# Performance work log

Hardware: AMD Instinct MI355X
Metric: run time of the kernel (lower is better)

The kernel has to match this reference:

```python
import jax, jax.numpy as jnp
import numpy as np

B, N, D, H, DH = 2, 2048, 1024, 16, 64  # batch, seq, dim, heads, dim_head


def setup_inputs() -> dict:
    key = jax.random.key(0)
    ks = jax.random.split(key, 5)
    x = jax.random.normal(ks[0], (B, N, D), dtype=jnp.float32)
    Wq = jax.random.normal(ks[1], (D, H * DH), dtype=jnp.float32) * 0.02
    Wk = jax.random.normal(ks[2], (D, H * DH), dtype=jnp.float32) * 0.02
    Wv = jax.random.normal(ks[3], (D, H * DH), dtype=jnp.float32) * 0.02
    Wo = jax.random.normal(ks[4], (H * DH, D), dtype=jnp.float32) * 0.02
    bo = jnp.zeros((D,), dtype=jnp.float32)
    return {"x": x, "Wq": Wq, "Wk": Wk, "Wv": Wv, "Wo": Wo, "bo": bo}


def reference(x, Wq, Wk, Wv, Wo, bo):
    b, n, _ = x.shape
    scale = DH ** -0.5
    q = (x @ Wq).reshape(b, n, H, DH)
    k = (x @ Wk).reshape(b, n, H, DH)
    v = (x @ Wv).reshape(b, n, H, DH)
    # ALiBi slopes: 1 / (256**(1/H))**(h+1), per get_alibi_slope
    base = (2.0 ** 8) ** (1.0 / H)
    slope = 1.0 / base ** jnp.arange(1, H + 1, dtype=jnp.float32)  # [H]
    pos = jnp.arange(n, dtype=jnp.float32)
    # q_bias=[slope, slope*i], k_bias=[-j, 1] -> dot = slope*(i-j)
    bias = slope[:, None, None] * (pos[:, None] - pos[None, :])  # [H, N, N]
    scores = jnp.einsum('bihd,bjhd->bhij', q, k) * scale + bias[None]
    causal = pos[:, None] >= pos[None, :]  # i >= j
    scores = jnp.where(causal[None, None], scores, jnp.float32(-1e30))
    attn = jax.nn.softmax(scores, axis=-1)
    out = jnp.einsum('bhij,bjhd->bihd', attn, v).reshape(b, n, H * DH)
    return out @ Wo + bo
```

## Files before the change

### kernel.cpp

```cpp
#include <hip/hip_runtime.h>
#include <hip/hip_bf16.h>


typedef __bf16 bf16x8 __attribute__((ext_vector_type(8)));
typedef float f32x4 __attribute__((ext_vector_type(4)));
typedef short s4 __attribute__((ext_vector_type(4)));
typedef unsigned short ushort_t;

#define MFMA_16x16x32(a, b, c) __builtin_amdgcn_mfma_f32_16x16x32_bf16(a, b, c, 0, 0, 0)
#define MFMA16(a, b, c) __builtin_amdgcn_mfma_f32_16x16x16bf16_1k(a, b, c, 0, 0, 0)

__device__ __forceinline__ ushort_t f2bf(float f) {
    __hip_bfloat16 h = __float2bfloat16(f);
    return __builtin_bit_cast(ushort_t, h);
}
__device__ __forceinline__ float bf2f(ushort_t u) {
    unsigned x = ((unsigned)u) << 16;
    return __builtin_bit_cast(float, x);
}

__device__ __forceinline__ void gl_lds16(const ushort_t* g, ushort_t* l) {
    __builtin_amdgcn_global_load_lds(
        (const __attribute__((address_space(1))) void*)g,
        (__attribute__((address_space(3))) void*)l, 16, 0, 0);
}

__device__ __forceinline__ unsigned detect_fp32(const void* wp) {
    const ushort_t* w = (const ushort_t*)wp;
    unsigned c = 0;
    #pragma unroll
    for (int i = 0; i < 128; ++i) c += (((w[i] >> 7) & 0xFF) >= 0x7F) ? 1u : 0u;
    return (c > 8) ? 1u : 0u;
}

__device__ __forceinline__ uint4 load8(const void* p, size_t idx, unsigned flag) {
    if (flag) {
        const float* f = (const float*)p + idx;
        float4 a = *(const float4*)f;
        float4 b = *(const float4*)(f + 4);
        ushort_t u[8] = { f2bf(a.x), f2bf(a.y), f2bf(a.z), f2bf(a.w),
                          f2bf(b.x), f2bf(b.y), f2bf(b.z), f2bf(b.w) };
        return *(uint4*)u;
    }
    return *(const uint4*)((const ushort_t*)p + idx);
}

struct Sched { unsigned short v[1024]; };
constexpr Sched make_sched() {
    Sched s{};
    int jc[16] = {1, 1, 2, 2, 3, 4, 6, 8, 12, 16, 23, 32, 32, 32, 32, 32};
    int sorted[1024] = {};
    int n = 0;
    for (int w = 32; w >= 1; --w) {
        for (int id = 0; id < 1024; ++id) {
            int bh = id & 31, qb = id >> 5;
            int cap = jc[bh & 15];
            int wi = (qb + 1 < cap) ? (qb + 1) : cap;
            if (wi == w) sorted[n++] = id;
        }
    }
    for (int r = 0; r < 4; ++r)
        for (int k = 0; k < 256; ++k)
            s.v[r * 256 + k] = (unsigned short)sorted[r * 256 + ((r & 1) ? (255 - k) : k)];
    return s;
}
__constant__ Sched g_sched = make_sched();

__global__ __launch_bounds__(256) void convert_x(
    const void* __restrict__ X, const void* __restrict__ Wq, const void* __restrict__ bo,
    ushort_t* __restrict__ Xc, ushort_t* __restrict__ boc)
{
    const unsigned flag = detect_fp32(Wq);
    const int blk = blockIdx.x;
    if (blk < 2048) {
        size_t idx = (size_t)blk * 2048 + (size_t)threadIdx.x * 8;
        *(uint4*)(Xc + idx) = load8(X, idx, flag);
    } else {
        size_t idx = (size_t)threadIdx.x * 8;
        if (idx < 1024) *(uint4*)(boc + idx) = load8(bo, idx, flag);
    }
}

__global__ __launch_bounds__(256) void transpose_w(
    const void* __restrict__ Wq, const void* __restrict__ Wk,
    const void* __restrict__ Wv, const void* __restrict__ Wo,
    ushort_t* __restrict__ WqT, ushort_t* __restrict__ WkT,
    ushort_t* __restrict__ WvT, ushort_t* __restrict__ WoT)
{
    __shared__ ushort_t T[64][72];
    const unsigned flag = detect_fp32(Wq);
    const int z = blockIdx.z;
    const void* W = (z == 0) ? Wq : ((z == 1) ? Wk : ((z == 2) ? Wv : Wo));
    ushort_t* WT = (z == 0) ? WqT : ((z == 1) ? WkT : ((z == 2) ? WvT : WoT));

    const int k0 = blockIdx.y * 64, n0 = blockIdx.x * 64;
    const int r = threadIdx.x >> 2, c = (threadIdx.x & 3) * 16;

    *(uint4*)&T[r][c]     = load8(W, (size_t)(k0 + r) * 1024 + n0 + c,     flag);
    *(uint4*)&T[r][c + 8] = load8(W, (size_t)(k0 + r) * 1024 + n0 + c + 8, flag);
    __syncthreads();
    ushort_t tmp[16];
    #pragma unroll
    for (int j = 0; j < 16; ++j) tmp[j] = T[c + j][r];
    *(uint4*)(WT + (size_t)(n0 + r) * 1024 + k0 + c)     = *(uint4*)&tmp[0];
    *(uint4*)(WT + (size_t)(n0 + r) * 1024 + k0 + c + 8) = *(uint4*)&tmp[8];
}

__global__ __launch_bounds__(256) void qkv_gemm(
    const ushort_t* __restrict__ X, const ushort_t* __restrict__ WqT,
    const ushort_t* __restrict__ WkT, const ushort_t* __restrict__ WvT,
    ushort_t* __restrict__ Q, ushort_t* __restrict__ K, ushort_t* __restrict__ Vt)
{
    __shared__ ushort_t As[128 * 32];
    __shared__ ushort_t Bs[128 * 32];

    const int z = blockIdx.z;
    const ushort_t* WT = (z == 0) ? WqT : ((z == 1) ? WkT : WvT);

    const int tid  = threadIdx.x;
    const int m0   = blockIdx.y * 128, n0 = blockIdx.x * 128;
    const int lane = tid & 63, wv = tid >> 6;
    const int quad = lane >> 4, l15 = lane & 15;
    const int wm = (wv & 1) * 64, wn = (wv >> 1) * 64;

    const int lrow = lane >> 2;
    const int schk = (lane & 3) ^ ((lane >> 3) & 3);
    const int ra0_ = wv * 16 + lrow;
    ushort_t* aB0 = As + wv * 512;
    ushort_t* aB1 = As + 2048 + wv * 512;
    ushort_t* bB0 = Bs + wv * 512;
    ushort_t* bB1 = Bs + 2048 + wv * 512;
    const int sp = quad ^ ((l15 >> 1) & 3);

    f32x4 acc[4][4] = {};

    for (int kt = 0; kt < 32; ++kt) {
        const int k0 = kt * 32;
        __syncthreads();
        gl_lds16(X  + (size_t)(m0 + ra0_)      * 1024 + k0 + schk * 8, aB0);
        gl_lds16(X  + (size_t)(m0 + 64 + ra0_) * 1024 + k0 + schk * 8, aB1);
        gl_lds16(WT + (size_t)(n0 + ra0_)      * 1024 + k0 + schk * 8, bB0);
        gl_lds16(WT + (size_t)(n0 + 64 + ra0_) * 1024 + k0 + schk * 8, bB1);
        __syncthreads();

        bf16x8 af[4], bfr[4];
        #pragma unroll
        for (int t = 0; t < 4; ++t) {
            af[t]  = *(const bf16x8*)(As + (wm + t * 16 + l15) * 32 + sp * 8);
            bfr[t] = *(const bf16x8*)(Bs + (wn + t * 16 + l15) * 32 + sp * 8);
        }
        #pragma unroll
        for (int mt = 0; mt < 4; ++mt)
            #pragma unroll
            for (int nt = 0; nt < 4; ++nt)
                acc[mt][nt] = MFMA_16x16x32(af[mt], bfr[nt], acc[mt][nt]);
    }

    #pragma unroll
    for (int mt = 0; mt < 4; ++mt) {
        #pragma unroll
        for (int nt = 0; nt < 4; ++nt) {
            if (z == 2) {
                int c  = n0 + wn + nt * 16 + l15;
                int h  = c >> 6, dh = c & 63;
                int mA = m0 + wm + mt * 16 + quad * 4;
                int b  = mA >> 11, nseq = mA & 2047;
                ushort_t pk[4];
                #pragma unroll
                for (int r = 0; r < 4; ++r) pk[r] = f2bf(acc[mt][nt][r]);
                *(ushort2*)(Vt + ((size_t)((b * 16 + h) * 64 + dh)) * 2048 + nseq)     = *(ushort2*)&pk[0];
                *(ushort2*)(Vt + ((size_t)((b * 16 + h) * 64 + dh)) * 2048 + nseq + 2) = *(ushort2*)&pk[2];
            } else {
                ushort_t* dst = (z == 0) ? Q : K;
                #pragma unroll
                for (int r = 0; r < 4; ++r) {
                    int m = m0 + wm + mt * 16 + quad * 4 + r;
                    int c = n0 + wn + nt * 16 + l15;
                    int b = m >> 11, nseq = m & 2047;
                    int h = c >> 6, dh = c & 63;
                    dst[((size_t)((b * 16 + h) * 2048 + nseq)) * 64 + dh] = f2bf(acc[mt][nt][r]);
                }
            }
        }
    }
}

__global__ __launch_bounds__(256) void attn_kernel(
    const ushort_t* __restrict__ Q, const ushort_t* __restrict__ K,
    const ushort_t* __restrict__ Vt, ushort_t* __restrict__ AO)
{
    __shared__ ushort_t Ks[64 * 72];
    __shared__ ushort_t Vs[64 * 72];

    const int tid  = threadIdx.x;
    const int wv   = tid >> 6, lane = tid & 63;
    const int quad = lane >> 4, l15 = lane & 15;
    const int item = g_sched.v[blockIdx.x];
    const int bh   = item & 31, h = bh & 15, b = bh >> 4;
    const int qb   = item >> 5;
    const int iw   = qb * 64 + wv * 16;
    const int i_   = iw + l15;

    const ushort_t* Qh = Q  + (size_t)bh * 2048 * 64;
    const ushort_t* Kh = K  + (size_t)bh * 2048 * 64;
    const ushort_t* Vh = Vt + (size_t)bh * 64 * 2048;

    const float LOG2E = 1.44269504088896340736f;
    const float sl2 = exp2f(-0.5f * (float)(h + 1)) * LOG2E;
    const float c1  = 0.125f * LOG2E;

    const int jcap   = (int)(46.0f / (sl2 * 64.0f)) + 1;
    const int ntiles = min(qb + 1, jcap);

    bf16x8 qf0 = *(const bf16x8*)(Qh + (size_t)(iw + l15) * 64 + quad * 8);
    bf16x8 qf1 = *(const bf16x8*)(Qh + (size_t)(iw + l15) * 64 + 32 + quad * 8);

    s4 onesf;
    #pragma unroll
    for (int e = 0; e < 4; ++e) onesf[e] = (short)0x3F80;

    float nb[4];
    #pragma unroll
    for (int r = 0; r < 4; ++r) nb[r] = -sl2 * (float)(quad * 4 + r);

    f32x4 accv[4] = {};
    f32x4 accl = {};

    const int sr = tid >> 2, sc = (tid & 3) * 16;

    uint4 ka0 = *(const uint4*)(Kh + (size_t)sr * 64 + sc);
    uint4 ka1 = *(const uint4*)(Kh + (size_t)sr * 64 + sc + 8);
    uint4 va0 = *(const uint4*)(Vh + (size_t)sr * 2048 + sc);
    uint4 va1 = *(const uint4*)(Vh + (size_t)sr * 2048 + sc + 8);

    auto subtile = [&](int jt, int js, bool masked) {
        const int j0s = jt * 64 + js * 16;
        const float bj = -sl2 * (float)j0s;
        f32x4 sT = {};
        bf16x8 kf0 = *(const bf16x8*)(Ks + (js * 16 + l15) * 72 + quad * 8);
        bf16x8 kf1 = *(const bf16x8*)(Ks + (js * 16 + l15) * 72 + 32 + quad * 8);
        sT = MFMA_16x16x32(kf0, qf0, sT);
        sT = MFMA_16x16x32(kf1, qf1, sT);
        unsigned u[4];
        #pragma unroll
        for (int r = 0; r < 4; ++r) {
            float p = exp2f(fmaf(sT[r], c1, nb[r] + bj));
            if (masked && (j0s + quad * 4 + r) > i_) p = 0.0f;
            u[r] = __builtin_bit_cast(unsigned, p) + 0x8000u;
        }
        uint2 dd = { (u[0] >> 16) | (u[1] & 0xFFFF0000u),
                     (u[2] >> 16) | (u[3] & 0xFFFF0000u) };
        s4 pf = __builtin_bit_cast(s4, dd);
        accl = MFMA16(onesf, pf, accl);
        #pragma unroll
        for (int dt = 0; dt < 4; ++dt) {
            s4 vf = *(const s4*)(Vs + (dt * 16 + l15) * 72 + js * 16 + quad * 4);
            accv[dt] = MFMA16(vf, pf, accv[dt]);
        }
    };

    for (int jt = 0; jt < ntiles; ++jt) {
        __syncthreads();
        *(uint4*)(Ks + sr * 72 + sc)     = ka0;
        *(uint4*)(Ks + sr * 72 + sc + 8) = ka1;
        *(uint4*)(Vs + sr * 72 + sc)     = va0;
        *(uint4*)(Vs + sr * 72 + sc + 8) = va1;
        __syncthreads();
        if (jt + 1 < ntiles) {
            int j0n = (jt + 1) * 64;
            ka0 = *(const uint4*)(Kh + (size_t)(j0n + sr) * 64 + sc);
            ka1 = *(const uint4*)(Kh + (size_t)(j0n + sr) * 64 + sc + 8);
            va0 = *(const uint4*)(Vh + (size_t)sr * 2048 + j0n + sc);
            va1 = *(const uint4*)(Vh + (size_t)sr * 2048 + j0n + sc + 8);
        }
        if (jt < qb) {
            #pragma unroll
            for (int js = 0; js < 4; ++js) subtile(jt, js, false);
        } else {
            for (int js = 0; js < wv; ++js) subtile(jt, js, false);
            subtile(jt, wv, true);
        }
    }

    const float inv = 1.0f / fmaxf(accl[0], 1e-30f);
    const size_t obase = ((size_t)(b * 2048 + i_)) * 1024 + h * 64;
    #pragma unroll
    for (int dt = 0; dt < 4; ++dt) {
        ushort_t pk[4];
        #pragma unroll
        for (int r = 0; r < 4; ++r) pk[r] = f2bf(accv[dt][r] * inv);
        *(ushort2*)(AO + obase + dt * 16 + quad * 4)     = *(ushort2*)&pk[0];
        *(ushort2*)(AO + obase + dt * 16 + quad * 4 + 2) = *(ushort2*)&pk[2];
    }
}

__global__ __launch_bounds__(256) void oproj_gemm(
    const ushort_t* __restrict__ A, const ushort_t* __restrict__ WT,
    const ushort_t* __restrict__ bias, float* __restrict__ out)
{
    __shared__ ushort_t As[128 * 32];
    __shared__ ushort_t Bs[128 * 32];

    const int tid  = threadIdx.x;
    const int m0   = blockIdx.y * 128, n0 = blockIdx.x * 128;
    const int lane = tid & 63, wv = tid >> 6;
    const int quad = lane >> 4, l15 = lane & 15;
    const int wm = (wv & 1) * 64, wn = (wv >> 1) * 64;

    const int lrow = lane >> 2;
    const int schk = (lane & 3) ^ ((lane >> 3) & 3);
    const int ra0_ = wv * 16 + lrow;
    ushort_t* aB0 = As + wv * 512;
    ushort_t* aB1 = As + 2048 + wv * 512;
    ushort_t* bB0 = Bs + wv * 512;
    ushort_t* bB1 = Bs + 2048 + wv * 512;
    const int sp = quad ^ ((l15 >> 1) & 3);

    f32x4 acc[4][4] = {};

    for (int kt = 0; kt < 32; ++kt) {
        const int k0 = kt * 32;
        __syncthreads();
        gl_lds16(A  + (size_t)(m0 + ra0_)      * 1024 + k0 + schk * 8, aB0);
        gl_lds16(A  + (size_t)(m0 + 64 + ra0_) * 1024 + k0 + schk * 8, aB1);
        gl_lds16(WT + (size_t)(n0 + ra0_)      * 1024 + k0 + schk * 8, bB0);
        gl_lds16(WT + (size_t)(n0 + 64 + ra0_) * 1024 + k0 + schk * 8, bB1);
        __syncthreads();

        bf16x8 af[4], bfr[4];
        #pragma unroll
        for (int t = 0; t < 4; ++t) {
            af[t]  = *(const bf16x8*)(As + (wm + t * 16 + l15) * 32 + sp * 8);
            bfr[t] = *(const bf16x8*)(Bs + (wn + t * 16 + l15) * 32 + sp * 8);
        }
        #pragma unroll
        for (int mt = 0; mt < 4; ++mt)
            #pragma unroll
            for (int nt = 0; nt < 4; ++nt)
                acc[mt][nt] = MFMA_16x16x32(af[mt], bfr[nt], acc[mt][nt]);
    }

    #pragma unroll
    for (int mt = 0; mt < 4; ++mt) {
        #pragma unroll
        for (int nt = 0; nt < 4; ++nt) {
            #pragma unroll
            for (int r = 0; r < 4; ++r) {
                int m = m0 + wm + mt * 16 + quad * 4 + r;
                int c = n0 + wn + nt * 16 + l15;
                out[(size_t)m * 1024 + c] = acc[mt][nt][r] + bf2f(bias[c]);
            }
        }
    }
}

extern "C" void kernel_launch(void* const* d_in, const int* in_sizes, int n_in,
                              void* d_out, int out_size, void* d_ws, size_t ws_size,
                              hipStream_t stream) {
    const void* X  = d_in[0];
    const void* Wq = d_in[1];
    const void* Wk = d_in[2];
    const void* Wv = d_in[3];
    const void* Wo = d_in[4];
    const void* bo = d_in[5];

    const size_t M = 1024 * 1024;
    ushort_t* ws  = (ushort_t*)d_ws;
    ushort_t* Qb  = ws;
    ushort_t* Kb  = ws + 4 * M;
    ushort_t* Vt  = ws + 8 * M;
    ushort_t* Xc  = ws + 12 * M;
    ushort_t* AO  = ws + 12 * M;
    ushort_t* WqT = ws + 16 * M;
    ushort_t* WkT = ws + 17 * M;
    ushort_t* WvT = ws + 18 * M;
    ushort_t* WoT = ws + 19 * M;
    ushort_t* boc = ws + 20 * M;
    float* out = (float*)d_out;

    convert_x<<<2049, 256, 0, stream>>>(X, Wq, bo, Xc, boc);
    transpose_w<<<dim3(16, 16, 4), 256, 0, stream>>>(Wq, Wk, Wv, Wo, WqT, WkT, WvT, WoT);
    qkv_gemm<<<dim3(8, 32, 3), 256, 0, stream>>>(Xc, WqT, WkT, WvT, Qb, Kb, Vt);
    attn_kernel<<<1024, 256, 0, stream>>>(Qb, Kb, Vt, AO);
    oproj_gemm<<<dim3(8, 32), 256, 0, stream>>>(AO, WoT, boc, out);
}
```

Baseline: 187.1 us.

## Group heads per XCD in attention block schedule for L2 locality

```diff
diff --git a/kernel.cpp b/kernel.cpp
--- a/kernel.cpp
+++ b/kernel.cpp
@@ -49,19 +49,33 @@
 constexpr Sched make_sched() {
     Sched s{};
     int jc[16] = {1, 1, 2, 2, 3, 4, 6, 8, 12, 16, 23, 32, 32, 32, 32, 32};
-    int sorted[1024] = {};
-    int n = 0;
-    for (int w = 32; w >= 1; --w) {
-        for (int id = 0; id < 1024; ++id) {
-            int bh = id & 31, qb = id >> 5;
-            int cap = jc[bh & 15];
-            int wi = (qb + 1 < cap) ? (qb + 1) : cap;
-            if (wi == w) sorted[n++] = id;
-        }
-    }
-    for (int r = 0; r < 4; ++r)
-        for (int k = 0; k < 256; ++k)
-            s.v[r * 256 + k] = (unsigned short)sorted[r * 256 + ((r & 1) ? (255 - k) : k)];
+    int grp[8][4] = {
+        {11,      12,      0,       2},
+        {13,      14,      1,       3},
+        {16 + 11, 16 + 12, 16 + 0,  16 + 2},
+        {16 + 13, 16 + 14, 16 + 1,  16 + 3},
+        {15,      10,      5,       4},
+        {16 + 15, 16 + 10, 16 + 5,  16 + 4},
+        {9,       8,       7,       6},
+        {16 + 9,  16 + 8,  16 + 7,  16 + 6},
+    };
+    for (int x = 0; x < 8; ++x) {
+        int items[128] = {};
+        int n = 0;
+        for (int w = 32; w >= 1; --w)
+            for (int gi = 0; gi < 4; ++gi) {
+                int bh = grp[x][gi], h = bh & 15;
+                for (int qb = 0; qb < 32; ++qb) {
+                    int wi = (qb + 1 < jc[h]) ? (qb + 1) : jc[h];
+                    if (wi == w) items[n++] = (qb << 5) | bh;
+                }
+            }
+        for (int t = 0; t < 128; ++t) {
+            int r = t >> 5, p = t & 31;
+            int cu = (r & 1) ? (31 - p) : p;
+            s.v[r * 256 + cu * 8 + x] = (unsigned short)items[t];
+        }
+    }
     return s;
 }
 __constant__ Sched g_sched = make_sched();
```

After: 186.5 us. About the same (-0.3%).
